# Performance work log

Measured on AMD Instinct MI355X. Metric: run time of the kernel, lower is better.

## Reference

```python
import jax, jax.numpy as jnp
import numpy as np

# Dims: batch, lig atoms (padded), rec residues, in-feat, heads, feat/head, edge-hid, n-edges
B, L, R, F, H, FH, FE, E = 16, 128, 512, 256, 8, 32, 64, 16384
HF = H * FH  # 256


def setup_inputs() -> dict:
    key = jax.random.key(0)
    ks = jax.random.split(key, 16)
    n = jax.random.normal
    return {
        "ll_feat": n(ks[0], (B, L, L, F), dtype=jnp.float32),
        "lig_feat": n(ks[1], (B, L, F), dtype=jnp.float32),
        "rec_feat": n(ks[2], (B, R, F), dtype=jnp.float32),
        "mask": jax.random.bernoulli(ks[3], 0.9, (B, L, L)),
        "e_batch": jax.random.randint(ks[4], (E,), 0, B),
        "e_src": jax.random.randint(ks[5], (E,), 0, L),
        "e_dst": jax.random.randint(ks[6], (E,), 0, L),
        # AttentionContract params: NormAndLinear (W,b + layernorm gamma/beta) + atn linear
        "Wc": n(ks[7], (HF, F)) * 0.05, "bc": jnp.zeros(HF), "gc": jnp.ones(HF), "bec": jnp.zeros(HF),
        "Wca": n(ks[8], (H, F)) * 0.05, "bca": jnp.zeros(H),
        # AttentionExpand params (x branch and y branch NormAndLinear)
        "Wex": n(ks[9], (HF, F)) * 0.05, "bex": jnp.zeros(HF), "gex": jnp.ones(HF), "beex": jnp.zeros(HF),
        "Wey": n(ks[10], (HF, F)) * 0.05, "bey": jnp.zeros(HF), "gey": jnp.ones(HF), "beey": jnp.zeros(HF),
        # edge projection (feat_to_edge_feat gather -> linear -> scatter)
        "We": n(ks[11], (FE, 2 * F)) * 0.05, "be": jnp.zeros(FE),
    }


def _norm_linear(x, W, b, g, beta):
    """NormAndLinear: linear(leaky_relu(x)) then layernorm over last dim."""
    h = jnp.einsum('...i,oi->...o', jax.nn.leaky_relu(x), W) + b
    mu = h.mean(-1, keepdims=True)
    var = ((h - mu) ** 2).mean(-1, keepdims=True)
    return g * (h - mu) * jax.lax.rsqrt(var + 1e-5) + beta


def _masked_softmax(x, mask, axis):
    """Faithful softmax_with_mask: exp(x-max), zero masked entries, /(sum+1e-10)."""
    xe = jnp.exp(x - x.max(axis=axis, keepdims=True))
    xe = jnp.where(mask, xe, 0.0)
    return xe / (xe.sum(axis=axis, keepdims=True) + 1e-10)


def reference(ll_feat, lig_feat, rec_feat, mask, e_batch, e_src, e_dst,
              Wc, bc, gc, bec, Wca, bca,
              Wex, bex, gex, beex, Wey, bey, gey, beey, We, be):
    # --- AttentionContract: (B,L,L,F) -> (B,L,H*FH), masked softmax over axis -3 (Y) ---
    of = _norm_linear(ll_feat, Wc, bc, gc, bec).reshape(B, L, L, H, FH)
    atn = (jnp.einsum('blyf,hf->blyh', jax.nn.leaky_relu(ll_feat), Wca) + bca)[..., None]  # (B,L,L,H,1)
    atn = _masked_softmax(atn, mask[..., None, None], axis=-3)
    contracted = (atn * of).sum(-3).reshape(B, L, HF)

    # --- AttentionExpand: (B,L,F),(B,R,F) -> (B,L,R,H) ---
    xf = _norm_linear(lig_feat, Wex, bex, gex, beex).reshape(B, L, H, FH)
    yf = _norm_linear(rec_feat, Wey, bey, gey, beey).reshape(B, R, H, FH)
    expanded = jnp.einsum('bxhf,byhf->bxyh', xf, yf)

    # --- feat_to_edge_feat gather + projection + lig_edges_to_ll_feat scatter ---
    ef = jnp.concatenate((lig_feat[e_batch, e_src], lig_feat[e_batch, e_dst]), axis=-1)  # (E,2F)
    ef = jax.nn.leaky_relu(ef @ We.T + be)  # (E,FE)
    llf = jnp.zeros((B, L, L, FE), ef.dtype).at[e_batch, e_src, e_dst].add(ef)

    return (contracted, expanded, llf)
```

## Files before the change

kernel.cpp:

```cpp
#include <hip/hip_runtime.h>
#include <cstdint>
#include <cstddef>

typedef unsigned int u32;
typedef unsigned short u16;
typedef __bf16 bf16x8 __attribute__((ext_vector_type(8)));
typedef float f32x16 __attribute__((ext_vector_type(16)));
typedef float f32x4v __attribute__((ext_vector_type(4)));

#define DEV static __device__ __forceinline__

DEV u16 f2bf(float f){ u32 u=__float_as_uint(f); return (u16)((u + 0x7FFFu + ((u>>16)&1u))>>16); }
DEV uint2 cvt4(float4 v){
  uint2 r;
  r.x = (u32)f2bf(v.x) | ((u32)f2bf(v.y)<<16);
  r.y = (u32)f2bf(v.z) | ((u32)f2bf(v.w)<<16);
  return r;
}
DEV uint2 cvt4(f32x4v v){
  uint2 r;
  r.x = (u32)f2bf(v.x) | ((u32)f2bf(v.y)<<16);
  r.y = (u32)f2bf(v.z) | ((u32)f2bf(v.w)<<16);
  return r;
}
DEV u32 lrelu_pk(u32 u){
  float lo=__uint_as_float(u<<16);
  float hi=__uint_as_float(u&0xFFFF0000u);
  lo=fmaxf(lo,0.01f*lo); hi=fmaxf(hi,0.01f*hi);
  return (u32)f2bf(lo) | (((u32)f2bf(hi))<<16);
}

__global__ void k_prepack(const float* __restrict__ Wc, const float* __restrict__ Wca,
    const float* __restrict__ Wex, const float* __restrict__ Wey, const float* __restrict__ We,
    const unsigned char* __restrict__ maskb,
    u16* __restrict__ wpc, u16* __restrict__ wpx, u16* __restrict__ wpy,
    u16* __restrict__ wpe, int* __restrict__ flags)
{
  int idx = blockIdx.x*256 + threadIdx.x;
  {
    int t=idx>>13, kk=(idx>>9)&15, ln=(idx>>3)&63, j=idx&7;
    int n=t*32+(ln&31), k=kk*16+(ln>>5)*8+j;
    if (idx < 73728){
      float v;
      if (t<8) v = Wc[n*256+k];
      else { int n2=n-256; v = (n2<8) ? Wca[n2*256+k] : 0.f; }
      wpc[idx]=f2bf(v);
    }
    if (idx < 65536){ wpx[idx]=f2bf(Wex[n*256+k]); wpy[idx]=f2bf(Wey[n*256+k]); }
  }
  if (idx < 32768){
    int t=idx>>14, kk=(idx>>9)&31, ln=(idx>>3)&63, j=idx&7;
    int n=t*32+(ln&31), k=kk*16+(ln>>5)*8+j;
    wpe[idx]=f2bf(We[n*512+k]);
  }
  if (idx==0){
    int c3f1=0,c3f3=0,nzoff=0,nz4m8=0,nz0=0;
    for (int i=0;i<256;i++){
      unsigned char b=maskb[i];
      if ((i&3)==1 && b==0x3F) c3f1++;
      if ((i&3)==3 && b==0x3F) c3f3++;
      if ((i&3)!=0 && b) nzoff++;
      if ((i&7)>=4 && b) nz4m8++;
      if ((i&7)==0 && b) nz0++;
    }
    int mode;
    if (c3f1>8) mode=2;
    else if (c3f3>8) mode=3;
    else if (nzoff>8) mode=0;
    else if (nz4m8==0 && nz0>4) mode=4;
    else mode=1;
    flags[0]=mode;
  }
}

__global__ __launch_bounds__(256,2) void k_contract(
    const float* __restrict__ ll, const void* __restrict__ maskp,
    const u16* __restrict__ Wp, const float* __restrict__ bc, const float* __restrict__ bca,
    const float* __restrict__ gc, const float* __restrict__ bec,
    const int* __restrict__ flags, float* __restrict__ outc)
{
  __shared__ __attribute__((aligned(16))) union SMem {
    char slab[65536];
    struct { float logit[1536]; float partial[1024]; } post;
  } sm;
  __shared__ float maskv[128];

  int tid=threadIdx.x, lane=tid&63, wave=tid>>6;
  int bl = blockIdx.x;
  const float* src = ll + (size_t)bl*(128*256);

  if (tid < 128){
    int mode = flags[0];
    size_t mi = (size_t)bl*128 + tid;
    bool on;
    if (mode==0)      on = ((const unsigned char*)maskp)[mi] != 0;
    else if (mode==1) on = ((const int*)maskp)[mi] != 0;
    else if (mode==2) on = ((const u16*)maskp)[mi] != 0;
    else if (mode==4) on = ((const unsigned long long*)maskp)[mi] != 0ull;
    else              on = (((const u32*)maskp)[mi]<<1) != 0;
    maskv[tid] = on ? 1.f : 0.f;
  }

  #pragma unroll 8
  for (int it=0;it<32;it++){
    int row = wave*32 + it;
    f32x4v v = __builtin_nontemporal_load((const f32x4v*)(src + row*256 + lane*4));
    uint2 pk = cvt4(v);
    *(uint2*)(sm.slab + row*512 + ((((lane>>1) ^ (row&31)))<<4) + (lane&1)*8) = pk;
  }
  __syncthreads();

  f32x16 acc[9];
  #pragma unroll
  for (int t=0;t<9;t++)
    #pragma unroll
    for (int i=0;i<16;i++) acc[t][i]=0.f;
  int y0 = wave*32;
  int arow = y0 + (lane&31);
  int axor = arow & 31;
  int half = lane>>5;
  const char* sb = sm.slab;
  const u16* wl = Wp + lane*8;

  uint4 raw = *(const uint4*)(sb + arow*512 + ((half ^ axor)<<4));
  bf16x8 w0 = *(const bf16x8*)(wl);
  bf16x8 w1 = *(const bf16x8*)(wl + 8192);
  bf16x8 w2 = *(const bf16x8*)(wl + 16384);
  bf16x8 w3 = *(const bf16x8*)(wl + 24576);
  bf16x8 w4 = *(const bf16x8*)(wl + 32768);
  bf16x8 w5 = *(const bf16x8*)(wl + 40960);
  bf16x8 w6 = *(const bf16x8*)(wl + 49152);
  bf16x8 w7 = *(const bf16x8*)(wl + 57344);
  bf16x8 w8 = *(const bf16x8*)(wl + 65536);

  #pragma unroll 4
  for (int kk=0;kk<16;kk++){
    int kn = (kk+1)&15;
    uint4 rawn = *(const uint4*)(sb + arow*512 + (((kn*2+half) ^ axor)<<4));
    const u16* wkn = wl + (size_t)kn*512;
    bf16x8 n0 = *(const bf16x8*)(wkn);
    bf16x8 n1 = *(const bf16x8*)(wkn + 8192);
    bf16x8 n2 = *(const bf16x8*)(wkn + 16384);
    bf16x8 n3 = *(const bf16x8*)(wkn + 24576);
    bf16x8 n4 = *(const bf16x8*)(wkn + 32768);
    bf16x8 n5 = *(const bf16x8*)(wkn + 40960);
    bf16x8 n6 = *(const bf16x8*)(wkn + 49152);
    bf16x8 n7 = *(const bf16x8*)(wkn + 57344);
    bf16x8 n8 = *(const bf16x8*)(wkn + 65536);
    __builtin_amdgcn_sched_barrier(0);
    uint4 t4; t4.x=lrelu_pk(raw.x); t4.y=lrelu_pk(raw.y); t4.z=lrelu_pk(raw.z); t4.w=lrelu_pk(raw.w);
    bf16x8 a = __builtin_bit_cast(bf16x8, t4);
    acc[0] = __builtin_amdgcn_mfma_f32_32x32x16_bf16(a, w0, acc[0], 0,0,0);
    acc[1] = __builtin_amdgcn_mfma_f32_32x32x16_bf16(a, w1, acc[1], 0,0,0);
    acc[2] = __builtin_amdgcn_mfma_f32_32x32x16_bf16(a, w2, acc[2], 0,0,0);
    acc[3] = __builtin_amdgcn_mfma_f32_32x32x16_bf16(a, w3, acc[3], 0,0,0);
    acc[4] = __builtin_amdgcn_mfma_f32_32x32x16_bf16(a, w4, acc[4], 0,0,0);
    acc[5] = __builtin_amdgcn_mfma_f32_32x32x16_bf16(a, w5, acc[5], 0,0,0);
    acc[6] = __builtin_amdgcn_mfma_f32_32x32x16_bf16(a, w6, acc[6], 0,0,0);
    acc[7] = __builtin_amdgcn_mfma_f32_32x32x16_bf16(a, w7, acc[7], 0,0,0);
    acc[8] = __builtin_amdgcn_mfma_f32_32x32x16_bf16(a, w8, acc[8], 0,0,0);
    raw=rawn;
    w0=n0; w1=n1; w2=n2; w3=n3; w4=n4; w5=n5; w6=n6; w7=n7; w8=n8;
  }
  __syncthreads();

  int col = lane & 31;
  float bv[8], gv[8], bev[8];
  #pragma unroll
  for (int t=0;t<8;t++){
    int n=t*32+col; bv[t]=bc[n]; gv[t]=gc[n]; bev[t]=bec[n];
  }
  float bcav = (col<8) ? bca[col] : 0.f;

  #pragma unroll
  for (int r=0;r<16;r++){
    int row=(r&3)+8*(r>>2)+4*half;
    float s=0.f, sq=0.f;
    #pragma unroll
    for (int t=0;t<8;t++){
      float v = acc[t][r] + bv[t]; acc[t][r]=v; s += v; sq = fmaf(v,v,sq);
    }
    #pragma unroll
    for (int m=1;m<=16;m<<=1){ s += __shfl_xor(s,m,64); sq += __shfl_xor(sq,m,64); }
    float mu = s*(1.f/256.f);
    float var = fmaf(sq,1.f/256.f, -mu*mu);
    float rin = rsqrtf(var+1e-5f);
    #pragma unroll
    for (int t=0;t<8;t++) acc[t][r] = fmaf((acc[t][r]-mu)*rin, gv[t], bev[t]);
    if (col<8) sm.post.logit[(y0+row)*12+col] = acc[8][r] + bcav;
  }
  __syncthreads();

  {
    int h = tid>>5, sub = tid&31;
    float lv[4], ev[4];
    #pragma unroll
    for (int j=0;j<4;j++) lv[j] = sm.post.logit[(sub+32*j)*12 + h];
    float mx = fmaxf(fmaxf(lv[0],lv[1]), fmaxf(lv[2],lv[3]));
    #pragma unroll
    for (int m=1;m<=16;m<<=1) mx = fmaxf(mx, __shfl_xor(mx,m,64));
    float ssum=0.f;
    #pragma unroll
    for (int j=0;j<4;j++){ ev[j] = __expf(lv[j]-mx)*maskv[sub+32*j]; ssum += ev[j]; }
    #pragma unroll
    for (int m=1;m<=16;m<<=1) ssum += __shfl_xor(ssum,m,64);
    float inv = 1.f/(ssum+1e-10f);
    #pragma unroll
    for (int j=0;j<4;j++) sm.post.logit[(sub+32*j)*12+h] = ev[j]*inv;
  }
  __syncthreads();

  float ctr[8];
  #pragma unroll
  for (int t=0;t<8;t++) ctr[t]=0.f;
  #pragma unroll
  for (int r=0;r<16;r++){
    int row=(r&3)+8*(r>>2)+4*half;
    const float* wr = &sm.post.logit[(y0+row)*12];
    float4 w0v = *(const float4*)wr;
    float4 w1v = *(const float4*)(wr+4);
    ctr[0]=fmaf(w0v.x,acc[0][r],ctr[0]); ctr[1]=fmaf(w0v.y,acc[1][r],ctr[1]);
    ctr[2]=fmaf(w0v.z,acc[2][r],ctr[2]); ctr[3]=fmaf(w0v.w,acc[3][r],ctr[3]);
    ctr[4]=fmaf(w1v.x,acc[4][r],ctr[4]); ctr[5]=fmaf(w1v.y,acc[5][r],ctr[5]);
    ctr[6]=fmaf(w1v.z,acc[6][r],ctr[6]); ctr[7]=fmaf(w1v.w,acc[7][r],ctr[7]);
  }
  #pragma unroll
  for (int t=0;t<8;t++) ctr[t] += __shfl_xor(ctr[t],32,64);
  if (lane<32){
    #pragma unroll
    for (int t=0;t<8;t++) sm.post.partial[wave*256 + t*32 + col] = ctr[t];
  }
  __syncthreads();
  float v = sm.post.partial[tid]+sm.post.partial[256+tid]
          + sm.post.partial[512+tid]+sm.post.partial[768+tid];
  outc[(size_t)bl*256 + tid] = v;
}

__global__ __launch_bounds__(256,2) void k_nl(
    const float* __restrict__ lig, const float* __restrict__ rec,
    const u16* __restrict__ Wpx, const u16* __restrict__ Wpy,
    const float* __restrict__ bx, const float* __restrict__ gx, const float* __restrict__ ex,
    const float* __restrict__ by, const float* __restrict__ gy, const float* __restrict__ ey,
    u16* __restrict__ xf, u16* __restrict__ yf)
{
  __shared__ __attribute__((aligned(16))) char slab[65536];
  int tid=threadIdx.x, lane=tid&63, wave=tid>>6;
  bool isx = blockIdx.x < 16;
  int bb = isx ? blockIdx.x : blockIdx.x - 16;
  const float* src  = isx ? lig : rec;
  const u16*  Wp    = isx ? Wpx : Wpy;
  const float* bias = isx ? bx : by;
  const float* g    = isx ? gx : gy;
  const float* beta = isx ? ex : ey;
  u16* dst          = isx ? xf : yf;

  const float* s0 = src + (size_t)bb*(128*256);
  #pragma unroll 8
  for (int it=0;it<32;it++){
    int row = wave*32 + it;
    float4 v = *(const float4*)(s0 + row*256 + lane*4);
    uint2 pk = cvt4(v);
    *(uint2*)(slab + row*512 + ((((lane>>1) ^ (row&31)))<<4) + (lane&1)*8) = pk;
  }
  __syncthreads();

  f32x16 acc[8];
  #pragma unroll
  for (int t=0;t<8;t++)
    #pragma unroll
    for (int i=0;i<16;i++) acc[t][i]=0.f;
  int y0 = wave*32;
  int arow = y0 + (lane&31);
  int axor = arow & 31;
  int half = lane>>5;
  const u16* wl = Wp + lane*8;

  uint4 raw = *(const uint4*)(slab + arow*512 + ((half ^ axor)<<4));
  bf16x8 w0 = *(const bf16x8*)(wl);
  bf16x8 w1 = *(const bf16x8*)(wl + 8192);
  bf16x8 w2 = *(const bf16x8*)(wl + 16384);
  bf16x8 w3 = *(const bf16x8*)(wl + 24576);
  bf16x8 w4 = *(const bf16x8*)(wl + 32768);
  bf16x8 w5 = *(const bf16x8*)(wl + 40960);
  bf16x8 w6 = *(const bf16x8*)(wl + 49152);
  bf16x8 w7 = *(const bf16x8*)(wl + 57344);

  #pragma unroll 4
  for (int kk=0;kk<16;kk++){
    int kn = (kk+1)&15;
    uint4 rawn = *(const uint4*)(slab + arow*512 + (((kn*2+half) ^ axor)<<4));
    const u16* wkn = wl + (size_t)kn*512;
    bf16x8 n0 = *(const bf16x8*)(wkn);
    bf16x8 n1 = *(const bf16x8*)(wkn + 8192);
    bf16x8 n2 = *(const bf16x8*)(wkn + 16384);
    bf16x8 n3 = *(const bf16x8*)(wkn + 24576);
    bf16x8 n4 = *(const bf16x8*)(wkn + 32768);
    bf16x8 n5 = *(const bf16x8*)(wkn + 40960);
    bf16x8 n6 = *(const bf16x8*)(wkn + 49152);
    bf16x8 n7 = *(const bf16x8*)(wkn + 57344);
    __builtin_amdgcn_sched_barrier(0);
    uint4 t4; t4.x=lrelu_pk(raw.x); t4.y=lrelu_pk(raw.y); t4.z=lrelu_pk(raw.z); t4.w=lrelu_pk(raw.w);
    bf16x8 a = __builtin_bit_cast(bf16x8, t4);
    acc[0] = __builtin_amdgcn_mfma_f32_32x32x16_bf16(a, w0, acc[0], 0,0,0);
    acc[1] = __builtin_amdgcn_mfma_f32_32x32x16_bf16(a, w1, acc[1], 0,0,0);
    acc[2] = __builtin_amdgcn_mfma_f32_32x32x16_bf16(a, w2, acc[2], 0,0,0);
    acc[3] = __builtin_amdgcn_mfma_f32_32x32x16_bf16(a, w3, acc[3], 0,0,0);
    acc[4] = __builtin_amdgcn_mfma_f32_32x32x16_bf16(a, w4, acc[4], 0,0,0);
    acc[5] = __builtin_amdgcn_mfma_f32_32x32x16_bf16(a, w5, acc[5], 0,0,0);
    acc[6] = __builtin_amdgcn_mfma_f32_32x32x16_bf16(a, w6, acc[6], 0,0,0);
    acc[7] = __builtin_amdgcn_mfma_f32_32x32x16_bf16(a, w7, acc[7], 0,0,0);
    raw=rawn;
    w0=n0; w1=n1; w2=n2; w3=n3; w4=n4; w5=n5; w6=n6; w7=n7;
  }
  int col = lane & 31;
  float bv[8], gv[8], bev[8];
  #pragma unroll
  for (int t=0;t<8;t++){
    int n=t*32+col; bv[t]=bias[n]; gv[t]=g[n]; bev[t]=beta[n];
  }
  #pragma unroll
  for (int r=0;r<16;r++){
    int row=(r&3)+8*(r>>2)+4*half;
    float s=0.f, sq=0.f;
    #pragma unroll
    for (int t=0;t<8;t++){
      float v = acc[t][r] + bv[t]; acc[t][r]=v; s += v; sq = fmaf(v,v,sq);
    }
    #pragma unroll
    for (int m=1;m<=16;m<<=1){ s += __shfl_xor(s,m,64); sq += __shfl_xor(sq,m,64); }
    float mu = s*(1.f/256.f);
    float var = fmaf(sq,1.f/256.f, -mu*mu);
    float rin = rsqrtf(var+1e-5f);
    size_t rowg = (size_t)bb*128 + y0 + row;
    #pragma unroll
    for (int t=0;t<8;t++){
      float v = fmaf((acc[t][r]-mu)*rin, gv[t], bev[t]);
      dst[rowg*256 + t*32 + col] = f2bf(v);
    }
  }
}

__global__ __launch_bounds__(256,2) void k_expand(
    const u16* __restrict__ xf, const u16* __restrict__ yf, float* __restrict__ oute)
{
  __shared__ __attribute__((aligned(16))) u16 ytile[32*264];
  __shared__ __attribute__((aligned(16))) float stage[4][2048];
  int tid=threadIdx.x, lane=tid&63, wave=tid>>6;
  int bi = blockIdx.x>>4, yt = blockIdx.x&15;

  #pragma unroll
  for (int i=0;i<4;i++){
    int idx=i*256+tid; int row=idx>>5, c=idx&31;
    uint4 v = *(const uint4*)(yf + ((size_t)(bi*512 + yt*32 + row))*256 + c*8);
    *(uint4*)((char*)ytile + row*528 + c*16) = v;
  }
  __syncthreads();

  bf16x8 af[2][8];
  #pragma unroll
  for (int xi=0;xi<2;xi++){
    int x = (wave*2+xi)*16 + (lane&15);
    #pragma unroll
    for (int h=0;h<8;h++)
      af[xi][h] = *(const bf16x8*)(xf + ((size_t)(bi*128+x))*256 + h*32 + (lane>>4)*8);
  }
  float* stw = stage[wave];
  #pragma unroll
  for (int xi=0;xi<2;xi++){
    #pragma unroll
    for (int nt=0;nt<2;nt++){
      f32x4v c[8];
      #pragma unroll
      for (int h=0;h<8;h++){
        bf16x8 bv = *(const bf16x8*)((const char*)ytile + (nt*16+(lane&15))*528 + (h*32+(lane>>4)*8)*2);
        f32x4v z = {0.f,0.f,0.f,0.f};
        c[h] = __builtin_amdgcn_mfma_f32_16x16x32_bf16(af[xi][h], bv, z, 0,0,0);
      }
      #pragma unroll
      for (int q=0;q<4;q++){
        int xp=(lane>>4)*4+q, yp=lane&15;
        float* sp = &stw[(xp*16+yp)*8];
        float4 v0; v0.x=c[0][q]; v0.y=c[1][q]; v0.z=c[2][q]; v0.w=c[3][q];
        float4 v1; v1.x=c[4][q]; v1.y=c[5][q]; v1.z=c[6][q]; v1.w=c[7][q];
        *(float4*)sp = v0;
        *(float4*)(sp+4) = v1;
      }
      #pragma unroll
      for (int j=0;j<4;j++){
        int pi=j*64+lane, xp=pi>>4, yp=pi&15;
        const float* sp = &stw[(xp*16+yp)*8];
        float4 a = *(const float4*)sp;
        float4 b2 = *(const float4*)(sp+4);
        size_t x=(size_t)(wave*2+xi)*16+xp, y=(size_t)yt*32+nt*16+yp;
        float* po = oute + (((size_t)bi*128+x)*512 + y)*8;
        *(float4*)po = a;
        *(float4*)(po+4) = b2;
      }
    }
  }
}

__global__ __launch_bounds__(128,1) void k_edges(
    const float* __restrict__ lig, const int* __restrict__ eb, const int* __restrict__ es,
    const int* __restrict__ ed, const u16* __restrict__ Wp, const float* __restrict__ bias,
    float* __restrict__ outl)
{
  __shared__ __attribute__((aligned(16))) char slab[65536];
  int tid=threadIdx.x, lane=tid&63, wave=tid>>6;
  int e0 = blockIdx.x*64;
  int ge = e0 + wave*32 + (lane&31);
  int b0=eb[ge], s0=es[ge], d0=ed[ge];
  long long ps = (long long)(uintptr_t)(lig + ((size_t)(b0*128+s0))*256);
  long long pd = (long long)(uintptr_t)(lig + ((size_t)(b0*128+d0))*256);
  #pragma unroll 4
  for (int i=0;i<32;i++){
    int ri = wave*32 + i;
    const float* sp = (const float*)(uintptr_t)__shfl(ps, i, 32);
    const float* dp = (const float*)(uintptr_t)__shfl(pd, i, 32);
    #pragma unroll
    for (int j=0;j<2;j++){
      const float* base = j ? dp : sp;
      float4 v = *(const float4*)(base + lane*4);
      uint2 pk = cvt4(v);
      int g = j*32 + (lane>>1);
      *(uint2*)(slab + (size_t)ri*1024 + ((g ^ (ri&63))<<4) + (lane&1)*8) = pk;
    }
  }
  __syncthreads();

  f32x16 acc[2];
  #pragma unroll
  for (int t=0;t<2;t++)
    #pragma unroll
    for (int i=0;i<16;i++) acc[t][i]=0.f;
  int arow = wave*32 + (lane&31);
  int axor = arow & 63;
  int half = lane>>5;
  const u16* wl = Wp + lane*8;

  uint4 raw0 = *(const uint4*)(slab + (size_t)arow*1024 + ((half ^ axor)<<4));
  uint4 raw1 = *(const uint4*)(slab + (size_t)arow*1024 + (((2+half) ^ axor)<<4));
  bf16x8 b00 = *(const bf16x8*)(wl);
  bf16x8 b01 = *(const bf16x8*)(wl + 16384);
  bf16x8 b10 = *(const bf16x8*)(wl + 512);
  bf16x8 b11 = *(const bf16x8*)(wl + 16896);

  for (int kk=0;kk<32;kk+=2){
    int kn = (kk+2)&31;
    uint4 r0n = *(const uint4*)(slab + (size_t)arow*1024 + (((kn*2+half) ^ axor)<<4));
    uint4 r1n = *(const uint4*)(slab + (size_t)arow*1024 + ((((kn+1)*2+half) ^ axor)<<4));
    const u16* wkn = wl + (size_t)kn*512;
    bf16x8 n00 = *(const bf16x8*)(wkn);
    bf16x8 n01 = *(const bf16x8*)(wkn + 16384);
    bf16x8 n10 = *(const bf16x8*)(wkn + 512);
    bf16x8 n11 = *(const bf16x8*)(wkn + 16896);
    __builtin_amdgcn_sched_barrier(0);
    bf16x8 a0 = __builtin_bit_cast(bf16x8, raw0);
    bf16x8 a1 = __builtin_bit_cast(bf16x8, raw1);
    acc[0] = __builtin_amdgcn_mfma_f32_32x32x16_bf16(a0, b00, acc[0], 0,0,0);
    acc[1] = __builtin_amdgcn_mfma_f32_32x32x16_bf16(a0, b01, acc[1], 0,0,0);
    acc[0] = __builtin_amdgcn_mfma_f32_32x32x16_bf16(a1, b10, acc[0], 0,0,0);
    acc[1] = __builtin_amdgcn_mfma_f32_32x32x16_bf16(a1, b11, acc[1], 0,0,0);
    raw0=r0n; raw1=r1n;
    b00=n00; b01=n01; b10=n10; b11=n11;
  }
  int col = lane&31;
  float bv0=bias[col], bv1=bias[32+col];
  #pragma unroll
  for (int r=0;r<16;r++){
    int row=(r&3)+8*(r>>2)+4*half;
    int ee = e0 + wave*32 + row;
    int bb=eb[ee], ss=es[ee], dd=ed[ee];
    float* cell = outl + (((size_t)(bb*128+ss))*128 + (size_t)dd)*64;
    #pragma unroll
    for (int t=0;t<2;t++){
      float v = acc[t][r] + (t ? bv1 : bv0);
      v = fmaxf(v, 0.01f*v);
      atomicAdd(cell + t*32 + col, v);
    }
  }
}

extern "C" void kernel_launch(void* const* d_in, const int* in_sizes, int n_in,
                              void* d_out, int out_size, void* d_ws, size_t ws_size,
                              hipStream_t stream)
{
  (void)in_sizes; (void)n_in; (void)out_size; (void)ws_size;
  const float* ll  = (const float*)d_in[0];
  const float* lig = (const float*)d_in[1];
  const float* rec = (const float*)d_in[2];
  const void* mask = d_in[3];
  const int* eb = (const int*)d_in[4];
  const int* es = (const int*)d_in[5];
  const int* ed = (const int*)d_in[6];
  const float* Wc  =(const float*)d_in[7];  const float* bc  =(const float*)d_in[8];
  const float* gc  =(const float*)d_in[9];  const float* bec =(const float*)d_in[10];
  const float* Wca =(const float*)d_in[11]; const float* bca =(const float*)d_in[12];
  const float* Wex =(const float*)d_in[13]; const float* bex =(const float*)d_in[14];
  const float* gex =(const float*)d_in[15]; const float* beex=(const float*)d_in[16];
  const float* Wey =(const float*)d_in[17]; const float* bey =(const float*)d_in[18];
  const float* gey =(const float*)d_in[19]; const float* beey=(const float*)d_in[20];
  const float* We  =(const float*)d_in[21]; const float* be  =(const float*)d_in[22];

  float* outc = (float*)d_out;
  float* oute = outc + 524288;
  float* outl = outc + 8912896;

  char* ws = (char*)d_ws;
  int* flags = (int*)ws;
  u16* wpc = (u16*)(ws + 4096);
  u16* wpx = (u16*)(ws + 151552);
  u16* wpy = (u16*)(ws + 282624);
  u16* wpe = (u16*)(ws + 413696);
  u16* xf  = (u16*)(ws + 479232);
  u16* yf  = (u16*)(ws + 1527808);

  hipLaunchKernelGGL(k_prepack, dim3(288), dim3(256), 0, stream,
                     Wc, Wca, Wex, Wey, We, (const unsigned char*)mask,
                     wpc, wpx, wpy, wpe, flags);
  (void)hipMemsetAsync(outl, 0, (size_t)16777216*4, stream);
  hipLaunchKernelGGL(k_nl, dim3(80), dim3(256), 0, stream,
                     lig, rec, wpx, wpy, bex, gex, beex, bey, gey, beey, xf, yf);
  hipLaunchKernelGGL(k_contract, dim3(2048), dim3(256), 0, stream,
                     ll, mask, wpc, bc, bca, gc, bec, flags, outc);
  hipLaunchKernelGGL(k_expand, dim3(256), dim3(256), 0, stream, xf, yf, oute);
  hipLaunchKernelGGL(k_edges, dim3(256), dim3(128), 0, stream, lig, eb, es, ed, wpe, be, outl);
}
```

Baseline: 533.4 us.

## Fuse contract, expand and edge kernels into one launch; zero output in prepack

Merges the contract, expand and edge-projection kernels into a single kernel that picks its work by block index, so the three phases share one launch and can overlap on the GPU. The separate memset of the edge output is replaced by a grid-stride zero loop inside the prepack kernel. The float-to-bf16 rounding now uses the hardware v_cvt_pk_bf16_f32 instruction instead of manual bit arithmetic. The edge phase is remapped to 256 threads with one 32-wide output tile per wave. The fused kernel uses the largest shared-memory footprint of the three for every block, and zeroing 64 MB in the small prepack grid may be slower than the memset.

```diff
diff --git a/kernel.cpp b/kernel.cpp
--- a/kernel.cpp
+++ b/kernel.cpp
@@ -11,30 +11,21 @@
 #define DEV static __device__ __forceinline__
 
 DEV u16 f2bf(float f){ u32 u=__float_as_uint(f); return (u16)((u + 0x7FFFu + ((u>>16)&1u))>>16); }
-DEV uint2 cvt4(float4 v){
-  uint2 r;
-  r.x = (u32)f2bf(v.x) | ((u32)f2bf(v.y)<<16);
-  r.y = (u32)f2bf(v.z) | ((u32)f2bf(v.w)<<16);
-  return r;
-}
-DEV uint2 cvt4(f32x4v v){
-  uint2 r;
-  r.x = (u32)f2bf(v.x) | ((u32)f2bf(v.y)<<16);
-  r.y = (u32)f2bf(v.z) | ((u32)f2bf(v.w)<<16);
-  return r;
-}
+DEV u32 cvtpk(float lo, float hi){ u32 r; asm("v_cvt_pk_bf16_f32 %0, %1, %2":"=v"(r):"v"(lo),"v"(hi)); return r; }
+DEV uint2 cvt4(float4 v){ uint2 r; r.x=cvtpk(v.x,v.y); r.y=cvtpk(v.z,v.w); return r; }
+DEV uint2 cvt4(f32x4v v){ uint2 r; r.x=cvtpk(v.x,v.y); r.y=cvtpk(v.z,v.w); return r; }
 DEV u32 lrelu_pk(u32 u){
   float lo=__uint_as_float(u<<16);
   float hi=__uint_as_float(u&0xFFFF0000u);
   lo=fmaxf(lo,0.01f*lo); hi=fmaxf(hi,0.01f*hi);
-  return (u32)f2bf(lo) | (((u32)f2bf(hi))<<16);
+  return cvtpk(lo,hi);
 }
 
 __global__ void k_prepack(const float* __restrict__ Wc, const float* __restrict__ Wca,
     const float* __restrict__ Wex, const float* __restrict__ Wey, const float* __restrict__ We,
     const unsigned char* __restrict__ maskb,
     u16* __restrict__ wpc, u16* __restrict__ wpx, u16* __restrict__ wpy,
-    u16* __restrict__ wpe, int* __restrict__ flags)
+    u16* __restrict__ wpe, int* __restrict__ flags, float* __restrict__ outl)
 {
   int idx = blockIdx.x*256 + threadIdx.x;
   {
@@ -53,6 +44,11 @@
     int n=t*32+(ln&31), k=kk*16+(ln>>5)*8+j;
     wpe[idx]=f2bf(We[n*512+k]);
   }
+  {
+    float4 z; z.x=0.f; z.y=0.f; z.z=0.f; z.w=0.f;
+    float4* p = (float4*)outl;
+    for (size_t i = (size_t)idx; i < 4194304u; i += 73728u) p[i] = z;
+  }
   if (idx==0){
     int c3f1=0,c3f3=0,nzoff=0,nz4m8=0,nz0=0;
     for (int i=0;i<256;i++){
@@ -73,20 +69,19 @@
   }
 }
 
-__global__ __launch_bounds__(256,2) void k_contract(
+union FMem {
+  struct { char slab[65536]; float maskv[128]; } c;
+  struct { u16 ytile[8448]; float stage[4][2048]; } e;
+  char eslab[65536];
+};
+
+DEV void contract_body(FMem& sm, int bl,
     const float* __restrict__ ll, const void* __restrict__ maskp,
     const u16* __restrict__ Wp, const float* __restrict__ bc, const float* __restrict__ bca,
     const float* __restrict__ gc, const float* __restrict__ bec,
     const int* __restrict__ flags, float* __restrict__ outc)
 {
-  __shared__ __attribute__((aligned(16))) union SMem {
-    char slab[65536];
-    struct { float logit[1536]; float partial[1024]; } post;
-  } sm;
-  __shared__ float maskv[128];
-
   int tid=threadIdx.x, lane=tid&63, wave=tid>>6;
-  int bl = blockIdx.x;
   const float* src = ll + (size_t)bl*(128*256);
 
   if (tid < 128){
@@ -98,7 +93,7 @@
     else if (mode==2) on = ((const u16*)maskp)[mi] != 0;
     else if (mode==4) on = ((const unsigned long long*)maskp)[mi] != 0ull;
     else              on = (((const u32*)maskp)[mi]<<1) != 0;
-    maskv[tid] = on ? 1.f : 0.f;
+    sm.c.maskv[tid] = on ? 1.f : 0.f;
   }
 
   #pragma unroll 8
@@ -106,7 +101,7 @@
     int row = wave*32 + it;
     f32x4v v = __builtin_nontemporal_load((const f32x4v*)(src + row*256 + lane*4));
     uint2 pk = cvt4(v);
-    *(uint2*)(sm.slab + row*512 + ((((lane>>1) ^ (row&31)))<<4) + (lane&1)*8) = pk;
+    *(uint2*)(sm.c.slab + row*512 + ((((lane>>1) ^ (row&31)))<<4) + (lane&1)*8) = pk;
   }
   __syncthreads();
 
@@ -119,7 +114,7 @@
   int arow = y0 + (lane&31);
   int axor = arow & 31;
   int half = lane>>5;
-  const char* sb = sm.slab;
+  const char* sb = sm.c.slab;
   const u16* wl = Wp + lane*8;
 
   uint4 raw = *(const uint4*)(sb + arow*512 + ((half ^ axor)<<4));
@@ -164,6 +159,9 @@
   }
   __syncthreads();
 
+  float* logit = (float*)sm.c.slab;
+  float* partial = logit + 1536;
+
   int col = lane & 31;
   float bv[8], gv[8], bev[8];
   #pragma unroll
@@ -187,7 +185,7 @@
     float rin = rsqrtf(var+1e-5f);
     #pragma unroll
     for (int t=0;t<8;t++) acc[t][r] = fmaf((acc[t][r]-mu)*rin, gv[t], bev[t]);
-    if (col<8) sm.post.logit[(y0+row)*12+col] = acc[8][r] + bcav;
+    if (col<8) logit[(y0+row)*12+col] = acc[8][r] + bcav;
   }
   __syncthreads();
 
@@ -195,18 +193,18 @@
     int h = tid>>5, sub = tid&31;
     float lv[4], ev[4];
     #pragma unroll
-    for (int j=0;j<4;j++) lv[j] = sm.post.logit[(sub+32*j)*12 + h];
+    for (int j=0;j<4;j++) lv[j] = logit[(sub+32*j)*12 + h];
     float mx = fmaxf(fmaxf(lv[0],lv[1]), fmaxf(lv[2],lv[3]));
     #pragma unroll
     for (int m=1;m<=16;m<<=1) mx = fmaxf(mx, __shfl_xor(mx,m,64));
     float ssum=0.f;
     #pragma unroll
-    for (int j=0;j<4;j++){ ev[j] = __expf(lv[j]-mx)*maskv[sub+32*j]; ssum += ev[j]; }
+    for (int j=0;j<4;j++){ ev[j] = __expf(lv[j]-mx)*sm.c.maskv[sub+32*j]; ssum += ev[j]; }
     #pragma unroll
     for (int m=1;m<=16;m<<=1) ssum += __shfl_xor(ssum,m,64);
     float inv = 1.f/(ssum+1e-10f);
     #pragma unroll
-    for (int j=0;j<4;j++) sm.post.logit[(sub+32*j)*12+h] = ev[j]*inv;
+    for (int j=0;j<4;j++) logit[(sub+32*j)*12+h] = ev[j]*inv;
   }
   __syncthreads();
 
@@ -216,7 +214,7 @@
   #pragma unroll
   for (int r=0;r<16;r++){
     int row=(r&3)+8*(r>>2)+4*half;
-    const float* wr = &sm.post.logit[(y0+row)*12];
+    const float* wr = &logit[(y0+row)*12];
     float4 w0v = *(const float4*)wr;
     float4 w1v = *(const float4*)(wr+4);
     ctr[0]=fmaf(w0v.x,acc[0][r],ctr[0]); ctr[1]=fmaf(w0v.y,acc[1][r],ctr[1]);
@@ -228,12 +226,148 @@
   for (int t=0;t<8;t++) ctr[t] += __shfl_xor(ctr[t],32,64);
   if (lane<32){
     #pragma unroll
-    for (int t=0;t<8;t++) sm.post.partial[wave*256 + t*32 + col] = ctr[t];
-  }
-  __syncthreads();
-  float v = sm.post.partial[tid]+sm.post.partial[256+tid]
-          + sm.post.partial[512+tid]+sm.post.partial[768+tid];
+    for (int t=0;t<8;t++) partial[wave*256 + t*32 + col] = ctr[t];
+  }
+  __syncthreads();
+  float v = partial[tid]+partial[256+tid]+partial[512+tid]+partial[768+tid];
   outc[(size_t)bl*256 + tid] = v;
+}
+
+DEV void expand_body(FMem& sm, int blk,
+    const u16* __restrict__ xf, const u16* __restrict__ yf, float* __restrict__ oute)
+{
+  int tid=threadIdx.x, lane=tid&63, wave=tid>>6;
+  int bi = blk>>4, yt = blk&15;
+
+  #pragma unroll
+  for (int i=0;i<4;i++){
+    int idx=i*256+tid; int row=idx>>5, c=idx&31;
+    uint4 v = *(const uint4*)(yf + ((size_t)(bi*512 + yt*32 + row))*256 + c*8);
+    *(uint4*)((char*)sm.e.ytile + row*528 + c*16) = v;
+  }
+  __syncthreads();
+
+  bf16x8 af[2][8];
+  #pragma unroll
+  for (int xi=0;xi<2;xi++){
+    int x = (wave*2+xi)*16 + (lane&15);
+    #pragma unroll
+    for (int h=0;h<8;h++)
+      af[xi][h] = *(const bf16x8*)(xf + ((size_t)(bi*128+x))*256 + h*32 + (lane>>4)*8);
+  }
+  float* stw = sm.e.stage[wave];
+  #pragma unroll
+  for (int xi=0;xi<2;xi++){
+    #pragma unroll
+    for (int nt=0;nt<2;nt++){
+      f32x4v c[8];
+      #pragma unroll
+      for (int h=0;h<8;h++){
+        bf16x8 bv = *(const bf16x8*)((const char*)sm.e.ytile + (nt*16+(lane&15))*528 + (h*32+(lane>>4)*8)*2);
+        f32x4v z = {0.f,0.f,0.f,0.f};
+        c[h] = __builtin_amdgcn_mfma_f32_16x16x32_bf16(af[xi][h], bv, z, 0,0,0);
+      }
+      #pragma unroll
+      for (int q=0;q<4;q++){
+        int xp=(lane>>4)*4+q, yp=lane&15;
+        float* sp = &stw[(xp*16+yp)*8];
+        float4 v0; v0.x=c[0][q]; v0.y=c[1][q]; v0.z=c[2][q]; v0.w=c[3][q];
+        float4 v1; v1.x=c[4][q]; v1.y=c[5][q]; v1.z=c[6][q]; v1.w=c[7][q];
+        *(float4*)sp = v0;
+        *(float4*)(sp+4) = v1;
+      }
+      #pragma unroll
+      for (int j=0;j<4;j++){
+        int pi=j*64+lane, xp=pi>>4, yp=pi&15;
+        const float* sp = &stw[(xp*16+yp)*8];
+        float4 a = *(const float4*)sp;
+        float4 b2 = *(const float4*)(sp+4);
+        size_t x=(size_t)(wave*2+xi)*16+xp, y=(size_t)yt*32+nt*16+yp;
+        float* po = oute + (((size_t)bi*128+x)*512 + y)*8;
+        *(float4*)po = a;
+        *(float4*)(po+4) = b2;
+      }
+    }
+  }
+}
+
+DEV void edges_body(FMem& sm, int blk,
+    const float* __restrict__ lig, const int* __restrict__ eb, const int* __restrict__ es,
+    const int* __restrict__ ed, const u16* __restrict__ Wp, const float* __restrict__ bias,
+    float* __restrict__ outl)
+{
+  char* slab = sm.eslab;
+  int tid=threadIdx.x, lane=tid&63, wave=tid>>6;
+  int e0 = blk*64;
+  int ge = e0 + wave*16 + (lane&15);
+  int b0=eb[ge], s0=es[ge], d0=ed[ge];
+  long long ps = (long long)(uintptr_t)(lig + ((size_t)(b0*128+s0))*256);
+  long long pd = (long long)(uintptr_t)(lig + ((size_t)(b0*128+d0))*256);
+  #pragma unroll 4
+  for (int i=0;i<16;i++){
+    int ri = wave*16 + i;
+    const float* sp = (const float*)(uintptr_t)__shfl(ps, i, 16);
+    const float* dp = (const float*)(uintptr_t)__shfl(pd, i, 16);
+    #pragma unroll
+    for (int j=0;j<2;j++){
+      const float* base = j ? dp : sp;
+      float4 v = *(const float4*)(base + lane*4);
+      uint2 pk = cvt4(v);
+      int g = j*32 + (lane>>1);
+      *(uint2*)(slab + (size_t)ri*1024 + ((g ^ (ri&63))<<4) + (lane&1)*8) = pk;
+    }
+  }
+  __syncthreads();
+
+  f32x16 acc;
+  #pragma unroll
+  for (int i=0;i<16;i++) acc[i]=0.f;
+  int arow = (wave&1)*32 + (lane&31);
+  int axor = arow & 63;
+  int half = lane>>5;
+  int t = wave>>1;
+  const u16* wl = Wp + lane*8 + (size_t)t*16384;
+
+  uint4 raw = *(const uint4*)(slab + (size_t)arow*1024 + ((half ^ axor)<<4));
+  bf16x8 w = *(const bf16x8*)(wl);
+  for (int kk=0;kk<32;kk++){
+    int kn = (kk+1)&31;
+    uint4 rn = *(const uint4*)(slab + (size_t)arow*1024 + (((kn*2+half) ^ axor)<<4));
+    bf16x8 nw = *(const bf16x8*)(wl + (size_t)kn*512);
+    __builtin_amdgcn_sched_barrier(0);
+    bf16x8 a = __builtin_bit_cast(bf16x8, raw);
+    acc = __builtin_amdgcn_mfma_f32_32x32x16_bf16(a, w, acc, 0,0,0);
+    raw=rn; w=nw;
+  }
+  int col = lane&31;
+  float bv = bias[t*32+col];
+  #pragma unroll
+  for (int r=0;r<16;r++){
+    int row=(r&3)+8*(r>>2)+4*half;
+    int ee = e0 + (wave&1)*32 + row;
+    int bb=eb[ee], ss=es[ee], dd=ed[ee];
+    float* cell = outl + (((size_t)(bb*128+ss))*128 + (size_t)dd)*64;
+    float v = acc[r] + bv;
+    v = fmaxf(v, 0.01f*v);
+    atomicAdd(cell + t*32 + col, v);
+  }
+}
+
+__global__ __launch_bounds__(256,2) void k_fused(
+    const float* __restrict__ ll, const void* __restrict__ maskp,
+    const u16* __restrict__ wpc, const float* __restrict__ bc, const float* __restrict__ bca,
+    const float* __restrict__ gc, const float* __restrict__ bec,
+    const int* __restrict__ flags, float* __restrict__ outc,
+    const u16* __restrict__ xf, const u16* __restrict__ yf, float* __restrict__ oute,
+    const float* __restrict__ lig, const int* __restrict__ eb, const int* __restrict__ es,
+    const int* __restrict__ ed, const u16* __restrict__ wpe, const float* __restrict__ be,
+    float* __restrict__ outl)
+{
+  __shared__ __attribute__((aligned(16))) FMem sm;
+  int bid = blockIdx.x;
+  if (bid < 256)       edges_body(sm, bid, lig, eb, es, ed, wpe, be, outl);
+  else if (bid < 512)  expand_body(sm, bid-256, xf, yf, oute);
+  else                 contract_body(sm, bid-512, ll, maskp, wpc, bc, bca, gc, bec, flags, outc);
 }
 
 __global__ __launch_bounds__(256,2) void k_nl(
@@ -340,147 +474,6 @@
   }
 }
 
-__global__ __launch_bounds__(256,2) void k_expand(
-    const u16* __restrict__ xf, const u16* __restrict__ yf, float* __restrict__ oute)
-{
-  __shared__ __attribute__((aligned(16))) u16 ytile[32*264];
-  __shared__ __attribute__((aligned(16))) float stage[4][2048];
-  int tid=threadIdx.x, lane=tid&63, wave=tid>>6;
-  int bi = blockIdx.x>>4, yt = blockIdx.x&15;
-
-  #pragma unroll
-  for (int i=0;i<4;i++){
-    int idx=i*256+tid; int row=idx>>5, c=idx&31;
-    uint4 v = *(const uint4*)(yf + ((size_t)(bi*512 + yt*32 + row))*256 + c*8);
-    *(uint4*)((char*)ytile + row*528 + c*16) = v;
-  }
-  __syncthreads();
-
-  bf16x8 af[2][8];
-  #pragma unroll
-  for (int xi=0;xi<2;xi++){
-    int x = (wave*2+xi)*16 + (lane&15);
-    #pragma unroll
-    for (int h=0;h<8;h++)
-      af[xi][h] = *(const bf16x8*)(xf + ((size_t)(bi*128+x))*256 + h*32 + (lane>>4)*8);
-  }
-  float* stw = stage[wave];
-  #pragma unroll
-  for (int xi=0;xi<2;xi++){
-    #pragma unroll
-    for (int nt=0;nt<2;nt++){
-      f32x4v c[8];
-      #pragma unroll
-      for (int h=0;h<8;h++){
-        bf16x8 bv = *(const bf16x8*)((const char*)ytile + (nt*16+(lane&15))*528 + (h*32+(lane>>4)*8)*2);
-        f32x4v z = {0.f,0.f,0.f,0.f};
-        c[h] = __builtin_amdgcn_mfma_f32_16x16x32_bf16(af[xi][h], bv, z, 0,0,0);
-      }
-      #pragma unroll
-      for (int q=0;q<4;q++){
-        int xp=(lane>>4)*4+q, yp=lane&15;
-        float* sp = &stw[(xp*16+yp)*8];
-        float4 v0; v0.x=c[0][q]; v0.y=c[1][q]; v0.z=c[2][q]; v0.w=c[3][q];
-        float4 v1; v1.x=c[4][q]; v1.y=c[5][q]; v1.z=c[6][q]; v1.w=c[7][q];
-        *(float4*)sp = v0;
-        *(float4*)(sp+4) = v1;
-      }
-      #pragma unroll
-      for (int j=0;j<4;j++){
-        int pi=j*64+lane, xp=pi>>4, yp=pi&15;
-        const float* sp = &stw[(xp*16+yp)*8];
-        float4 a = *(const float4*)sp;
-        float4 b2 = *(const float4*)(sp+4);
-        size_t x=(size_t)(wave*2+xi)*16+xp, y=(size_t)yt*32+nt*16+yp;
-        float* po = oute + (((size_t)bi*128+x)*512 + y)*8;
-        *(float4*)po = a;
-        *(float4*)(po+4) = b2;
-      }
-    }
-  }
-}
-
-__global__ __launch_bounds__(128,1) void k_edges(
-    const float* __restrict__ lig, const int* __restrict__ eb, const int* __restrict__ es,
-    const int* __restrict__ ed, const u16* __restrict__ Wp, const float* __restrict__ bias,
-    float* __restrict__ outl)
-{
-  __shared__ __attribute__((aligned(16))) char slab[65536];
-  int tid=threadIdx.x, lane=tid&63, wave=tid>>6;
-  int e0 = blockIdx.x*64;
-  int ge = e0 + wave*32 + (lane&31);
-  int b0=eb[ge], s0=es[ge], d0=ed[ge];
-  long long ps = (long long)(uintptr_t)(lig + ((size_t)(b0*128+s0))*256);
-  long long pd = (long long)(uintptr_t)(lig + ((size_t)(b0*128+d0))*256);
-  #pragma unroll 4
-  for (int i=0;i<32;i++){
-    int ri = wave*32 + i;
-    const float* sp = (const float*)(uintptr_t)__shfl(ps, i, 32);
-    const float* dp = (const float*)(uintptr_t)__shfl(pd, i, 32);
-    #pragma unroll
-    for (int j=0;j<2;j++){
-      const float* base = j ? dp : sp;
-      float4 v = *(const float4*)(base + lane*4);
-      uint2 pk = cvt4(v);
-      int g = j*32 + (lane>>1);
-      *(uint2*)(slab + (size_t)ri*1024 + ((g ^ (ri&63))<<4) + (lane&1)*8) = pk;
-    }
-  }
-  __syncthreads();
-
-  f32x16 acc[2];
-  #pragma unroll
-  for (int t=0;t<2;t++)
-    #pragma unroll
-    for (int i=0;i<16;i++) acc[t][i]=0.f;
-  int arow = wave*32 + (lane&31);
-  int axor = arow & 63;
-  int half = lane>>5;
-  const u16* wl = Wp + lane*8;
-
-  uint4 raw0 = *(const uint4*)(slab + (size_t)arow*1024 + ((half ^ axor)<<4));
-  uint4 raw1 = *(const uint4*)(slab + (size_t)arow*1024 + (((2+half) ^ axor)<<4));
-  bf16x8 b00 = *(const bf16x8*)(wl);
-  bf16x8 b01 = *(const bf16x8*)(wl + 16384);
-  bf16x8 b10 = *(const bf16x8*)(wl + 512);
-  bf16x8 b11 = *(const bf16x8*)(wl + 16896);
-
-  for (int kk=0;kk<32;kk+=2){
-    int kn = (kk+2)&31;
-    uint4 r0n = *(const uint4*)(slab + (size_t)arow*1024 + (((kn*2+half) ^ axor)<<4));
-    uint4 r1n = *(const uint4*)(slab + (size_t)arow*1024 + ((((kn+1)*2+half) ^ axor)<<4));
-    const u16* wkn = wl + (size_t)kn*512;
-    bf16x8 n00 = *(const bf16x8*)(wkn);
-    bf16x8 n01 = *(const bf16x8*)(wkn + 16384);
-    bf16x8 n10 = *(const bf16x8*)(wkn + 512);
-    bf16x8 n11 = *(const bf16x8*)(wkn + 16896);
-    __builtin_amdgcn_sched_barrier(0);
-    bf16x8 a0 = __builtin_bit_cast(bf16x8, raw0);
-    bf16x8 a1 = __builtin_bit_cast(bf16x8, raw1);
-    acc[0] = __builtin_amdgcn_mfma_f32_32x32x16_bf16(a0, b00, acc[0], 0,0,0);
-    acc[1] = __builtin_amdgcn_mfma_f32_32x32x16_bf16(a0, b01, acc[1], 0,0,0);
-    acc[0] = __builtin_amdgcn_mfma_f32_32x32x16_bf16(a1, b10, acc[0], 0,0,0);
-    acc[1] = __builtin_amdgcn_mfma_f32_32x32x16_bf16(a1, b11, acc[1], 0,0,0);
-    raw0=r0n; raw1=r1n;
-    b00=n00; b01=n01; b10=n10; b11=n11;
-  }
-  int col = lane&31;
-  float bv0=bias[col], bv1=bias[32+col];
-  #pragma unroll
-  for (int r=0;r<16;r++){
-    int row=(r&3)+8*(r>>2)+4*half;
-    int ee = e0 + wave*32 + row;
-    int bb=eb[ee], ss=es[ee], dd=ed[ee];
-    float* cell = outl + (((size_t)(bb*128+ss))*128 + (size_t)dd)*64;
-    #pragma unroll
-    for (int t=0;t<2;t++){
-      float v = acc[t][r] + (t ? bv1 : bv0);
-      v = fmaxf(v, 0.01f*v);
-      atomicAdd(cell + t*32 + col, v);
-    }
-  }
-}
-
 extern "C" void kernel_launch(void* const* d_in, const int* in_sizes, int n_in,
                               void* d_out, int out_size, void* d_ws, size_t ws_size,
                               hipStream_t stream)
@@ -517,12 +510,10 @@
 
   hipLaunchKernelGGL(k_prepack, dim3(288), dim3(256), 0, stream,
                      Wc, Wca, Wex, Wey, We, (const unsigned char*)mask,
-                     wpc, wpx, wpy, wpe, flags);
-  (void)hipMemsetAsync(outl, 0, (size_t)16777216*4, stream);
+                     wpc, wpx, wpy, wpe, flags, outl);
   hipLaunchKernelGGL(k_nl, dim3(80), dim3(256), 0, stream,
                      lig, rec, wpx, wpy, bex, gex, beex, bey, gey, beey, xf, yf);
-  hipLaunchKernelGGL(k_contract, dim3(2048), dim3(256), 0, stream,
-                     ll, mask, wpc, bc, bca, gc, bec, flags, outc);
-  hipLaunchKernelGGL(k_expand, dim3(256), dim3(256), 0, stream, xf, yf, oute);
-  hipLaunchKernelGGL(k_edges, dim3(256), dim3(128), 0, stream, lig, eb, es, ed, wpe, be, outl);
-}
+  hipLaunchKernelGGL(k_fused, dim3(2560), dim3(256), 0, stream,
+                     ll, mask, wpc, bc, bca, gc, bec, flags, outc,
+                     xf, yf, oute, lig, eb, es, ed, wpe, be, outl);
+}
```

Result: faster. 504.0 us (median of 2 runs) (-5.5%).
